# Performance work log

Hardware: AMD Instinct MI355X
Metric: run time of the kernel (lower is better)

## Reference

```python
import jax, jax.numpy as jnp
import numpy as np

HEADS = 16
DIM_HEAD = 64
SCALE = DIM_HEAD ** -0.5
EPS = 1e-5


def setup_inputs() -> dict:
    key = jax.random.key(0)
    ks = jax.random.split(key, 4)
    B, S, D = 2, 2048, 1024
    x = jax.random.normal(ks[0], (B, S, D), dtype=jnp.float32)
    gamma = jnp.ones((D,), dtype=jnp.float32)
    beta = jnp.zeros((D,), dtype=jnp.float32)
    w_qkv = jax.random.normal(ks[1], (D, 3 * D), dtype=jnp.float32) * (D ** -0.5)
    w_out = jax.random.normal(ks[2], (D, D), dtype=jnp.float32) * (D ** -0.5)
    b_out = jnp.zeros((D,), dtype=jnp.float32)
    return {"x": x, "gamma": gamma, "beta": beta, "w_qkv": w_qkv,
            "w_out": w_out, "b_out": b_out}


def reference(x, gamma, beta, w_qkv, w_out, b_out):
    B, S, D = x.shape
    # pre-attention LayerNorm (matches triton layernorm kernel math)
    mean = jnp.mean(x, axis=-1, keepdims=True)
    centered = x - mean
    var = jnp.mean(centered * centered, axis=-1, keepdims=True)
    xn = centered * jax.lax.rsqrt(var + EPS) * gamma + beta
    # qkv projection (no bias), split into heads: b s (h d) -> b h s d
    qkv = xn @ w_qkv  # [B, S, 3D]
    q, k, v = jnp.split(qkv, 3, axis=-1)
    split_heads = lambda t: t.reshape(B, S, HEADS, DIM_HEAD).transpose(0, 2, 1, 3)
    q, k, v = split_heads(q) * SCALE, split_heads(k), split_heads(v)
    # unfused attention: full [B,H,S,S] scores, row softmax, then AV
    sim = jnp.einsum('bhid,bhjd->bhij', q, k)
    attn = jax.nn.softmax(sim, axis=-1)
    out = jnp.einsum('bhij,bhjd->bhid', attn, v)
    out = out.transpose(0, 2, 1, 3).reshape(B, S, D)  # merge heads
    return out @ w_out + b_out
```

## Files before the change

### kernel.cpp

```cpp
#include <hip/hip_runtime.h>
#include <hip/hip_bf16.h>

constexpr int Dm = 1024;
constexpr int Sq = 2048;
constexpr int Hh = 16;
constexpr int Dh = 64;
constexpr int Rows = 4096;

typedef __attribute__((ext_vector_type(8))) short bf16x8;
typedef __attribute__((ext_vector_type(8))) _Float16 f16x8;
typedef __attribute__((ext_vector_type(4))) float f32x4;
typedef __attribute__((ext_vector_type(16))) float f32x16;
typedef unsigned short u16;

__device__ inline u16 f2bf(float f) {
  union { float f; unsigned int u; } v; v.f = f;
  unsigned int r = v.u + 0x7FFFu + ((v.u >> 16) & 1u);
  return (u16)(r >> 16);
}
__device__ inline float bf2f(u16 h) {
  union { unsigned int u; float f; } v; v.u = (unsigned int)h << 16;
  return v.f;
}
__device__ inline unsigned int pack2(float a, float b) {
  return (unsigned int)f2bf(a) | ((unsigned int)f2bf(b) << 16);
}
__device__ inline u16 f2h(float f) {
  union { _Float16 h; u16 u; } v; v.h = (_Float16)f;
  return v.u;
}
__device__ inline float h2f(u16 h) {
  union { u16 u; _Float16 h; } v; v.u = h;
  return (float)v.h;
}
__device__ inline unsigned int pack2h(float a, float b) {
  return (unsigned int)f2h(a) | ((unsigned int)f2h(b) << 16);
}
__device__ inline int pkbf(float lo, float hi) {
  float2 f = {lo, hi};
  __hip_bfloat162 h = __float22bfloat162_rn(f);
  union { __hip_bfloat162 h; int i; } u; u.h = h;
  return u.i;
}
__device__ __forceinline__ void gload16(u16* lds, const u16* g) {
  __builtin_amdgcn_global_load_lds(
      (const __attribute__((address_space(1))) unsigned int*)g,
      (__attribute__((address_space(3))) unsigned int*)lds, 16, 0, 0);
}

template <int BASE>
__device__ inline void mk_frag(const f32x16 s, const int half, int dw[4]) {
  int p0 = pkbf(s[BASE + 0], s[BASE + 1]);
  int p1 = pkbf(s[BASE + 2], s[BASE + 3]);
  int p2 = pkbf(s[BASE + 4], s[BASE + 5]);
  int p3 = pkbf(s[BASE + 6], s[BASE + 7]);
  int t0 = half ? p0 : p2, t1 = half ? p1 : p3;
  int u0 = __shfl_xor(t0, 32), u1 = __shfl_xor(t1, 32);
  dw[0] = half ? u0 : p0;
  dw[1] = half ? u1 : p1;
  dw[2] = half ? p2 : u0;
  dw[3] = half ? p3 : u1;
}

__device__ inline float tsum32(const f32x16 a, const f32x16 b) {
  float t[16];
#pragma unroll
  for (int j = 0; j < 16; ++j) t[j] = a[j] + b[j];
#pragma unroll
  for (int w = 8; w >= 1; w >>= 1)
#pragma unroll
    for (int j = 0; j < 8; ++j)
      if (j < w) t[j] = t[j] + t[j + w];
  return t[0];
}

__global__ __launch_bounds__(256) void ln_kernel(
    const float* __restrict__ x, const float* __restrict__ gamma,
    const float* __restrict__ beta, u16* __restrict__ xh) {
  const int row = blockIdx.x;
  const int t = threadIdx.x;
  float4 v = reinterpret_cast<const float4*>(x + (size_t)row * Dm)[t];
  float s = v.x + v.y + v.z + v.w;
  float s2 = v.x * v.x + v.y * v.y + v.z * v.z + v.w * v.w;
#pragma unroll
  for (int off = 32; off > 0; off >>= 1) {
    s += __shfl_down(s, off);
    s2 += __shfl_down(s2, off);
  }
  __shared__ float red[8];
  if ((t & 63) == 0) { red[t >> 6] = s; red[(t >> 6) + 4] = s2; }
  __syncthreads();
  float ts = red[0] + red[1] + red[2] + red[3];
  float ts2 = red[4] + red[5] + red[6] + red[7];
  float mean = ts * (1.0f / Dm);
  float var = ts2 * (1.0f / Dm) - mean * mean;
  float rstd = rsqrtf(var + 1e-5f);
  float4 g = reinterpret_cast<const float4*>(gamma)[t];
  float4 b = reinterpret_cast<const float4*>(beta)[t];
  float o0 = (v.x - mean) * rstd * g.x + b.x;
  float o1 = (v.y - mean) * rstd * g.y + b.y;
  float o2 = (v.z - mean) * rstd * g.z + b.z;
  float o3 = (v.w - mean) * rstd * g.w + b.w;
  uint2 hw = {pack2h(o0, o1), pack2h(o2, o3)};
  *reinterpret_cast<uint2*>(xh + (size_t)row * Dm + t * 4) = hw;
}

__global__ __launch_bounds__(256) void convert_w(
    const float* __restrict__ w, u16* __restrict__ wh, int N) {
  __shared__ float T[64][65];
  const int n0 = blockIdx.x * 64, k0 = blockIdx.y * 64;
  const int t = threadIdx.x;
#pragma unroll
  for (int p = 0; p < 4; ++p) {
    int fid = p * 256 + t;
    int kr = fid >> 4, nn = (fid & 15) * 4;
    float4 v = *reinterpret_cast<const float4*>(w + (size_t)(k0 + kr) * N + n0 + nn);
    T[kr][nn] = v.x; T[kr][nn + 1] = v.y; T[kr][nn + 2] = v.z; T[kr][nn + 3] = v.w;
  }
  __syncthreads();
  const int n = t >> 2, kc = (t & 3) * 16;
  unsigned int hw[8];
#pragma unroll
  for (int i = 0; i < 8; ++i)
    hw[i] = pack2h(T[kc + 2 * i][n], T[kc + 2 * i + 1][n]);
  size_t o = (size_t)(n0 + n) * 1024 + k0 + kc;
  *reinterpret_cast<uint4*>(wh + o) = *reinterpret_cast<uint4*>(&hw[0]);
  *reinterpret_cast<uint4*>(wh + o + 8) = *reinterpret_cast<uint4*>(&hw[4]);
}

template <int BM, int BN, int N, int MODE, int NBN, int NWG, int SPLIT>
__global__ __launch_bounds__(256) void gemm_mfma(
    const u16* __restrict__ Ahg, const u16* __restrict__ Alg,
    const u16* __restrict__ Bhg,
    float* __restrict__ oF, u16* __restrict__ qq, u16* __restrict__ kk,
    u16* __restrict__ vv, const float* __restrict__ bias) {
  constexpr int MF = BM / 32;
  constexpr int NF = BN / 32;
  constexpr int AI = BM / 64;
  constexpr int BI = BN / 64;
  __shared__ __align__(16) u16 Ah[2][BM * 32], Bh[2][BN * 32];
  __shared__ __align__(16) u16 Al[2][SPLIT ? BM * 32 : 8];
  const int tid = threadIdx.x;
  const int wgid = (blockIdx.x & 7) * (NWG / 8) + (blockIdx.x >> 3);
  const int bn = wgid % NBN, bm = wgid / NBN;
  const int wv = tid >> 6, lane = tid & 63;
  const int qn = lane & 15, g = lane >> 4;
  const int wr = wv >> 1, wc = wv & 1;
  const int m0 = bm * BM, n0 = bn * BN;
  const int r4 = lane >> 2, c4 = lane & 3;
  const int c4s = c4 ^ ((r4 >> 1) & 3);
  const int gs = g ^ ((qn >> 1) & 3);

  f32x4 acc[MF][NF];
#pragma unroll
  for (int m = 0; m < MF; ++m)
#pragma unroll
    for (int n = 0; n < NF; ++n) acc[m][n] = (f32x4){0.f, 0.f, 0.f, 0.f};

  auto stage = [&](int bf, int kt2) {
    const int k0 = kt2 * 32;
#pragma unroll
    for (int j = 0; j < AI; ++j) {
      const int sl = wv * AI + j;
      const size_t go = (size_t)(m0 + sl * 16 + r4) * Dm + k0 + c4s * 8;
      gload16(&Ah[bf][sl * 512], Ahg + go);
      if constexpr (SPLIT) gload16(&Al[bf][sl * 512], Alg + go);
    }
#pragma unroll
    for (int j = 0; j < BI; ++j) {
      const int sl = wv * BI + j;
      const size_t go = (size_t)(n0 + sl * 16 + r4) * Dm + k0 + c4s * 8;
      gload16(&Bh[bf][sl * 512], Bhg + go);
    }
  };

  stage(0, 0);
  __syncthreads();
  int buf = 0;

  for (int kt = 0; kt < Dm / 32; ++kt) {
    if (kt + 1 < Dm / 32) stage(buf ^ 1, kt + 1);
    f16x8 af0[MF], af1[MF], bb[NF];
#pragma unroll
    for (int m = 0; m < MF; ++m) {
      const int ro = (wr * (BM / 2) + m * 16 + qn) * 32 + gs * 8;
      af0[m] = *reinterpret_cast<const f16x8*>(&Ah[buf][ro]);
      if constexpr (SPLIT) af1[m] = *reinterpret_cast<const f16x8*>(&Al[buf][ro]);
    }
#pragma unroll
    for (int n = 0; n < NF; ++n) {
      const int ro = (wc * (BN / 2) + n * 16 + qn) * 32 + gs * 8;
      bb[n] = *reinterpret_cast<const f16x8*>(&Bh[buf][ro]);
    }
    __builtin_amdgcn_s_setprio(1);
#pragma unroll
    for (int m = 0; m < MF; ++m)
#pragma unroll
      for (int n = 0; n < NF; ++n) {
        acc[m][n] = __builtin_amdgcn_mfma_f32_16x16x32_f16(af0[m], bb[n], acc[m][n], 0, 0, 0);
        if constexpr (SPLIT)
          acc[m][n] = __builtin_amdgcn_mfma_f32_16x16x32_f16(af1[m], bb[n], acc[m][n], 0, 0, 0);
      }
    __builtin_amdgcn_s_setprio(0);
    __syncthreads();
    buf ^= 1;
  }

  if (MODE == 0) {
    const int which = n0 >> 10;
#pragma unroll
    for (int n = 0; n < NF; ++n) {
      const int c = n0 + wc * (BN / 2) + n * 16 + qn;
      const int d = c & 1023, h = d >> 6, dh = d & 63;
#pragma unroll
      for (int m = 0; m < MF; ++m) {
        const int mr0 = m0 + wr * (BM / 2) + m * 16 + 4 * g;
        const int bb2 = mr0 >> 11, ss = mr0 & 2047;
        if (which == 2) {
          uint2 w = {pack2(acc[m][n][0], acc[m][n][1]),
                     pack2(acc[m][n][2], acc[m][n][3])};
          *reinterpret_cast<uint2*>(&vv[(((size_t)bb2 * Hh + h) * Dh + dh) * Sq + ss]) = w;
        } else {
          u16* dst = (which == 0) ? qq : kk;
          const float sc = (which == 0) ? 0.125f * 1.44269504089f : 1.0f;
#pragma unroll
          for (int r = 0; r < 4; ++r)
            dst[(((size_t)bb2 * Hh + h) * Sq + (ss + r)) * Dh + dh] =
                f2bf(acc[m][n][r] * sc);
        }
      }
    }
  } else {
#pragma unroll
    for (int n = 0; n < NF; ++n) {
      const int c = n0 + wc * (BN / 2) + n * 16 + qn;
      const float bv = bias[c];
#pragma unroll
      for (int m = 0; m < MF; ++m) {
        const int mr0 = m0 + wr * (BM / 2) + m * 16 + 4 * g;
#pragma unroll
        for (int r = 0; r < 4; ++r)
          oF[(size_t)(mr0 + r) * N + c] = acc[m][n][r] + bv;
      }
    }
  }
}

__global__ __launch_bounds__(256, 2) void attn_lds(
    const u16* __restrict__ Q, const u16* __restrict__ K,
    const u16* __restrict__ Vt, u16* __restrict__ Oh, u16* __restrict__ Ol) {
  __shared__ __align__(16) u16 Ksh[2][8192];
  __shared__ __align__(16) u16 Vsh[2][8192];
  const int tid = threadIdx.x;
  const int wv = tid >> 6, lane = tid & 63;
  const int ln31 = lane & 31, half = lane >> 5;
  const int n = (blockIdx.x & 7) * 64 + (blockIdx.x >> 3);
  const int bh = n >> 4, qt = n & 15;
  const int q0 = qt * 128 + wv * 32;
  const u16* Qb = Q + ((size_t)bh * Sq + q0) * Dh;
  const u16* Kb = K + (size_t)bh * Sq * Dh;
  const u16* Vb = Vt + (size_t)bh * Dh * Sq;

  auto stage = [&](int bufi, int kt2) {
    if (wv < 2) {
#pragma unroll
      for (int j = 0; j < 8; ++j) {
        const int sl = wv * 8 + j;
        const int r = sl * 8 + (lane >> 3);
        const int c2 = (lane & 7) ^ (r & 7);
        gload16(&Ksh[bufi][sl * 512], Kb + (size_t)(kt2 * 128 + r) * Dh + c2 * 8);
      }
    } else {
#pragma unroll
      for (int j = 0; j < 8; ++j) {
        const int sl = (wv - 2) * 8 + j;
        const int r = sl * 4 + (lane >> 4);
        const int c2 = (lane & 15) ^ (r & 15);
        gload16(&Vsh[bufi][sl * 512], Vb + (size_t)r * Sq + kt2 * 128 + c2 * 8);
      }
    }
  };

  bf16x8 qf[4];
#pragma unroll
  for (int c = 0; c < 4; ++c)
    qf[c] = *reinterpret_cast<const bf16x8*>(Qb + ln31 * Dh + c * 16 + 8 * half);

  f32x16 o0, o1;
#pragma unroll
  for (int j = 0; j < 16; ++j) { o0[j] = 0.f; o1[j] = 0.f; }
  float lrun = 0.f;

  stage(0, 0);
  __syncthreads();
  int buf = 0;

  for (int kt2 = 0; kt2 < 16; ++kt2) {
    if (kt2 + 1 < 16) stage(buf ^ 1, kt2 + 1);
#pragma unroll
    for (int h = 0; h < 2; ++h) {
      bf16x8 kf[2][4];
#pragma unroll
      for (int sub = 0; sub < 2; ++sub)
#pragma unroll
        for (int c = 0; c < 4; ++c) {
          const int row = h * 64 + sub * 32 + ln31;
          kf[sub][c] = *reinterpret_cast<const bf16x8*>(
              &Ksh[buf][row * 64 + (((2 * c + half) ^ (row & 7)) << 3)]);
        }
      f32x16 s0, s1;
#pragma unroll
      for (int j = 0; j < 16; ++j) { s0[j] = 0.f; s1[j] = 0.f; }
      __builtin_amdgcn_s_setprio(1);
#pragma unroll
      for (int c = 0; c < 4; ++c) {
        s0 = __builtin_amdgcn_mfma_f32_32x32x16_bf16(kf[0][c], qf[c], s0, 0, 0, 0);
        s1 = __builtin_amdgcn_mfma_f32_32x32x16_bf16(kf[1][c], qf[c], s1, 0, 0, 0);
      }
      __builtin_amdgcn_s_setprio(0);
      bf16x8 vf[2][4];
#pragma unroll
      for (int h2 = 0; h2 < 2; ++h2)
#pragma unroll
        for (int c = 0; c < 4; ++c) {
          const int row = h2 * 32 + ln31;
          const int ch = (h * 8 + 2 * c + half) ^ (row & 15);
          vf[h2][c] = *reinterpret_cast<const bf16x8*>(
              &Vsh[buf][row * 128 + (ch << 3)]);
        }
#pragma unroll
      for (int j = 0; j < 16; ++j) s0[j] = __builtin_amdgcn_exp2f(s0[j]);
#pragma unroll
      for (int j = 0; j < 16; ++j) s1[j] = __builtin_amdgcn_exp2f(s1[j]);
      float sum = tsum32(s0, s1);
      sum += __shfl_xor(sum, 32);
      lrun += sum;
      int dw[4][4];
      mk_frag<0>(s0, half, dw[0]);
      mk_frag<8>(s0, half, dw[1]);
      mk_frag<0>(s1, half, dw[2]);
      mk_frag<8>(s1, half, dw[3]);
      __builtin_amdgcn_s_setprio(1);
#pragma unroll
      for (int c = 0; c < 4; ++c) {
        union { int4 i; bf16x8 b; } u;
        u.i = make_int4(dw[c][0], dw[c][1], dw[c][2], dw[c][3]);
        o0 = __builtin_amdgcn_mfma_f32_32x32x16_bf16(vf[0][c], u.b, o0, 0, 0, 0);
        o1 = __builtin_amdgcn_mfma_f32_32x32x16_bf16(vf[1][c], u.b, o1, 0, 0, 0);
      }
      __builtin_amdgcn_s_setprio(0);
    }
    __syncthreads();
    buf ^= 1;
  }

  const float inv = 1.0f / lrun;
  const int b = bh >> 4, hh = bh & 15;
  u16* oph = Oh + ((size_t)(b * Sq) + q0 + ln31) * Dm + hh * 64;
  u16* opl = Ol + ((size_t)(b * Sq) + q0 + ln31) * Dm + hh * 64;
#pragma unroll
  for (int h2 = 0; h2 < 2; ++h2) {
#pragma unroll
    for (int rg = 0; rg < 4; ++rg) {
      const int dh = h2 * 32 + 8 * rg + 4 * half;
      float v0, v1, v2, v3;
      if (h2 == 0) {
        v0 = o0[4 * rg] * inv; v1 = o0[4 * rg + 1] * inv;
        v2 = o0[4 * rg + 2] * inv; v3 = o0[4 * rg + 3] * inv;
      } else {
        v0 = o1[4 * rg] * inv; v1 = o1[4 * rg + 1] * inv;
        v2 = o1[4 * rg + 2] * inv; v3 = o1[4 * rg + 3] * inv;
      }
      u16 h0 = f2h(v0), h1 = f2h(v1), h2b = f2h(v2), h3 = f2h(v3);
      uint2 hw = {(unsigned)h0 | ((unsigned)h1 << 16),
                  (unsigned)h2b | ((unsigned)h3 << 16)};
      uint2 lw = {pack2h(v0 - h2f(h0), v1 - h2f(h1)),
                  pack2h(v2 - h2f(h2b), v3 - h2f(h3))};
      *reinterpret_cast<uint2*>(oph + dh) = hw;
      *reinterpret_cast<uint2*>(opl + dh) = lw;
    }
  }
}

extern "C" void kernel_launch(void* const* d_in, const int* in_sizes, int n_in,
                              void* d_out, int out_size, void* d_ws, size_t ws_size,
                              hipStream_t stream) {
  const float* x = (const float*)d_in[0];
  const float* gamma = (const float*)d_in[1];
  const float* beta = (const float*)d_in[2];
  const float* w_qkv = (const float*)d_in[3];
  const float* w_out = (const float*)d_in[4];
  const float* b_out = (const float*)d_in[5];
  float* out = (float*)d_out;
  u16* W = (u16*)d_ws;
  const size_t NT = (size_t)Rows * Dm;
  const size_t MT = (size_t)Dm * Dm;
  u16* xh = W;
  u16* Qbf = W + NT;
  u16* Kbf = W + 2 * NT;
  u16* Vbf = W + 3 * NT;
  u16* Ohh = W + 4 * NT;
  u16* Oll = W + 5 * NT;
  u16* wqh = W + 6 * NT;
  u16* woh = wqh + 3 * MT;

  convert_w<<<dim3(48, 16), dim3(256), 0, stream>>>(w_qkv, wqh, 3072);
  convert_w<<<dim3(16, 16), dim3(256), 0, stream>>>(w_out, woh, 1024);
  ln_kernel<<<dim3(Rows), dim3(256), 0, stream>>>(x, gamma, beta, xh);
  gemm_mfma<128, 128, 3072, 0, 24, 768, 0><<<dim3(768), dim3(256), 0, stream>>>(
      xh, nullptr, wqh, nullptr, Qbf, Kbf, Vbf, nullptr);
  attn_lds<<<dim3(512), dim3(256), 0, stream>>>(Qbf, Kbf, Vbf, Ohh, Oll);
  gemm_mfma<128, 64, 1024, 1, 16, 512, 1><<<dim3(512), dim3(256), 0, stream>>>(
      Ohh, Oll, woh, out, nullptr, nullptr, nullptr, b_out);
}
```

Baseline: 141.1 us.

## Compute softmax row sums via MFMA and drop hi/lo split of attention output

Replaces the per-lane VALU tree reduction and cross-lane shuffle for the softmax denominator with an extra MFMA against an all-ones bf16 matrix, accumulating row sums on the matrix cores. It also stops writing a low-order fp16 residual of the attention output and switches the output projection GEMM to a single-operand path, halving the output writes and the A-operand reads in that GEMM. The cost is one more MFMA per chunk, and the loss of the hi/lo compensation lowers output precision. The row sum is also now taken from the bf16-rounded probabilities rather than the fp32 values.

Result: faster. 130.0 us, median of 2 (-7.8%).

```diff
diff --git a/kernel.cpp b/kernel.cpp
--- a/kernel.cpp
+++ b/kernel.cpp
@@ -18,20 +18,12 @@
   unsigned int r = v.u + 0x7FFFu + ((v.u >> 16) & 1u);
   return (u16)(r >> 16);
 }
-__device__ inline float bf2f(u16 h) {
-  union { unsigned int u; float f; } v; v.u = (unsigned int)h << 16;
-  return v.f;
-}
 __device__ inline unsigned int pack2(float a, float b) {
   return (unsigned int)f2bf(a) | ((unsigned int)f2bf(b) << 16);
 }
 __device__ inline u16 f2h(float f) {
   union { _Float16 h; u16 u; } v; v.h = (_Float16)f;
   return v.u;
-}
-__device__ inline float h2f(u16 h) {
-  union { u16 u; _Float16 h; } v; v.u = h;
-  return (float)v.h;
 }
 __device__ inline unsigned int pack2h(float a, float b) {
   return (unsigned int)f2h(a) | ((unsigned int)f2h(b) << 16);
@@ -60,18 +52,6 @@
   dw[1] = half ? u1 : p1;
   dw[2] = half ? p2 : u0;
   dw[3] = half ? p3 : u1;
-}
-
-__device__ inline float tsum32(const f32x16 a, const f32x16 b) {
-  float t[16];
-#pragma unroll
-  for (int j = 0; j < 16; ++j) t[j] = a[j] + b[j];
-#pragma unroll
-  for (int w = 8; w >= 1; w >>= 1)
-#pragma unroll
-    for (int j = 0; j < 8; ++j)
-      if (j < w) t[j] = t[j] + t[j + w];
-  return t[0];
 }
 
 __global__ __launch_bounds__(256) void ln_kernel(
@@ -248,7 +228,7 @@
 
 __global__ __launch_bounds__(256, 2) void attn_lds(
     const u16* __restrict__ Q, const u16* __restrict__ K,
-    const u16* __restrict__ Vt, u16* __restrict__ Oh, u16* __restrict__ Ol) {
+    const u16* __restrict__ Vt, u16* __restrict__ Oh) {
   __shared__ __align__(16) u16 Ksh[2][8192];
   __shared__ __align__(16) u16 Vsh[2][8192];
   const int tid = threadIdx.x;
@@ -286,10 +266,12 @@
   for (int c = 0; c < 4; ++c)
     qf[c] = *reinterpret_cast<const bf16x8*>(Qb + ln31 * Dh + c * 16 + 8 * half);
 
-  f32x16 o0, o1;
-#pragma unroll
-  for (int j = 0; j < 16; ++j) { o0[j] = 0.f; o1[j] = 0.f; }
-  float lrun = 0.f;
+  union { int4 i; bf16x8 b; } ones;
+  ones.i = make_int4(0x3F803F80, 0x3F803F80, 0x3F803F80, 0x3F803F80);
+
+  f32x16 o0, o1, lacc;
+#pragma unroll
+  for (int j = 0; j < 16; ++j) { o0[j] = 0.f; o1[j] = 0.f; lacc[j] = 0.f; }
 
   stage(0, 0);
   __syncthreads();
@@ -332,9 +314,6 @@
       for (int j = 0; j < 16; ++j) s0[j] = __builtin_amdgcn_exp2f(s0[j]);
 #pragma unroll
       for (int j = 0; j < 16; ++j) s1[j] = __builtin_amdgcn_exp2f(s1[j]);
-      float sum = tsum32(s0, s1);
-      sum += __shfl_xor(sum, 32);
-      lrun += sum;
       int dw[4][4];
       mk_frag<0>(s0, half, dw[0]);
       mk_frag<8>(s0, half, dw[1]);
@@ -347,6 +326,7 @@
         u.i = make_int4(dw[c][0], dw[c][1], dw[c][2], dw[c][3]);
         o0 = __builtin_amdgcn_mfma_f32_32x32x16_bf16(vf[0][c], u.b, o0, 0, 0, 0);
         o1 = __builtin_amdgcn_mfma_f32_32x32x16_bf16(vf[1][c], u.b, o1, 0, 0, 0);
+        lacc = __builtin_amdgcn_mfma_f32_32x32x16_bf16(ones.b, u.b, lacc, 0, 0, 0);
       }
       __builtin_amdgcn_s_setprio(0);
     }
@@ -354,10 +334,9 @@
     buf ^= 1;
   }
 
-  const float inv = 1.0f / lrun;
+  const float inv = 1.0f / lacc[0];
   const int b = bh >> 4, hh = bh & 15;
   u16* oph = Oh + ((size_t)(b * Sq) + q0 + ln31) * Dm + hh * 64;
-  u16* opl = Ol + ((size_t)(b * Sq) + q0 + ln31) * Dm + hh * 64;
 #pragma unroll
   for (int h2 = 0; h2 < 2; ++h2) {
 #pragma unroll
@@ -371,13 +350,8 @@
         v0 = o1[4 * rg] * inv; v1 = o1[4 * rg + 1] * inv;
         v2 = o1[4 * rg + 2] * inv; v3 = o1[4 * rg + 3] * inv;
       }
-      u16 h0 = f2h(v0), h1 = f2h(v1), h2b = f2h(v2), h3 = f2h(v3);
-      uint2 hw = {(unsigned)h0 | ((unsigned)h1 << 16),
-                  (unsigned)h2b | ((unsigned)h3 << 16)};
-      uint2 lw = {pack2h(v0 - h2f(h0), v1 - h2f(h1)),
-                  pack2h(v2 - h2f(h2b), v3 - h2f(h3))};
+      uint2 hw = {pack2h(v0, v1), pack2h(v2, v3)};
       *reinterpret_cast<uint2*>(oph + dh) = hw;
-      *reinterpret_cast<uint2*>(opl + dh) = lw;
     }
   }
 }
@@ -400,8 +374,7 @@
   u16* Kbf = W + 2 * NT;
   u16* Vbf = W + 3 * NT;
   u16* Ohh = W + 4 * NT;
-  u16* Oll = W + 5 * NT;
-  u16* wqh = W + 6 * NT;
+  u16* wqh = W + 5 * NT;
   u16* woh = wqh + 3 * MT;
 
   convert_w<<<dim3(48, 16), dim3(256), 0, stream>>>(w_qkv, wqh, 3072);
@@ -409,7 +382,7 @@
   ln_kernel<<<dim3(Rows), dim3(256), 0, stream>>>(x, gamma, beta, xh);
   gemm_mfma<128, 128, 3072, 0, 24, 768, 0><<<dim3(768), dim3(256), 0, stream>>>(
       xh, nullptr, wqh, nullptr, Qbf, Kbf, Vbf, nullptr);
-  attn_lds<<<dim3(512), dim3(256), 0, stream>>>(Qbf, Kbf, Vbf, Ohh, Oll);
-  gemm_mfma<128, 64, 1024, 1, 16, 512, 1><<<dim3(512), dim3(256), 0, stream>>>(
-      Ohh, Oll, woh, out, nullptr, nullptr, nullptr, b_out);
-}
+  attn_lds<<<dim3(512), dim3(256), 0, stream>>>(Qbf, Kbf, Vbf, Ohh);
+  gemm_mfma<128, 64, 1024, 1, 16, 512, 0><<<dim3(512), dim3(256), 0, stream>>>(
+      Ohh, nullptr, woh, out, nullptr, nullptr, nullptr, b_out);
+}
```
